# Kernel optimization log

Measured on AMD Instinct MI355X. Metric: run time of the kernel, lower is better.

The kernel has to match this reference:

```python
import jax, jax.numpy as jnp
import numpy as np
from jax import lax

N_THETAS = 16
N_RHOS = 5
N_BINS = N_THETAS * N_RHOS  # 80
N_FEAT = 4
N_ROT = 16
MAX_RHO = 12.0
EPS = 1e-5
N_SAMPLES = 4096
N_VERT = 128


def _initial_coords():
    grid_rho = np.linspace(0.0, MAX_RHO, num=N_RHOS + 1)[1:]
    grid_theta = np.linspace(0.0, 2 * np.pi, num=N_THETAS + 1)[:-1]
    gr, gt = np.meshgrid(grid_rho, grid_theta, sparse=False)
    gr = gr.T.flatten().astype(np.float32)  # [80]
    gt = gt.T.flatten().astype(np.float32)  # [80]
    return gr, gt


def setup_inputs() -> dict:
    key = jax.random.key(0)
    k1, k2, k3, k4, k5 = jax.random.split(key, 5)
    rho_coords = jax.random.uniform(k1, (N_SAMPLES, N_VERT), jnp.float32) * MAX_RHO
    theta_coords = jax.random.uniform(k2, (N_SAMPLES, N_VERT), jnp.float32) * (2 * np.pi)
    input_feat = jax.random.normal(k3, (N_SAMPLES, N_VERT, N_FEAT), jnp.float32)
    mask = (jax.random.uniform(k4, (N_SAMPLES, N_VERT, 1), jnp.float32) < 0.9).astype(jnp.float32)
    gr, gt = _initial_coords()
    mu_rho = jnp.tile(jnp.asarray(gr)[None, None, :], (N_FEAT, 1, 1))       # [F,1,80]
    mu_theta = jnp.tile(jnp.asarray(gt)[None, None, :], (N_FEAT, 1, 1))     # [F,1,80]
    sigma_rho = jnp.full((N_FEAT, 1, N_BINS), MAX_RHO / 8.0, jnp.float32)
    sigma_theta = jnp.ones((N_FEAT, 1, N_BINS), jnp.float32)
    # VarianceScaling(fan_avg, uniform) for square [80,80]: limit = sqrt(3/80)
    limit = np.sqrt(3.0 / N_BINS)
    W_conv = jax.random.uniform(k5, (N_FEAT, N_BINS, N_BINS), jnp.float32, -limit, limit)
    b_conv = jnp.zeros((N_FEAT, N_BINS), jnp.float32)
    return {
        "rho_coords": rho_coords, "theta_coords": theta_coords,
        "input_feat": input_feat, "mask": mask,
        "mu_rho": mu_rho, "sigma_rho": sigma_rho,
        "mu_theta": mu_theta, "sigma_theta": sigma_theta,
        "W_conv": W_conv, "b_conv": b_conv,
    }


def _geodesic_conv(rho_coords, theta_coords, input_feat, mask,
                   mu_rho, sigma_rho, mu_theta, sigma_theta, W_conv, b_conv):
    two_pi = jnp.float32(2 * np.pi)
    rot_step = two_pi / N_ROT
    outs = []
    for i in range(N_FEAT):  # small, structurally distinct feature channels
        feat = input_feat[:, :, i]  # [N,V]
        # rho Gaussian is rotation-independent: [N,V,80]
        rho_g = jnp.exp(-jnp.square(rho_coords[..., None] - mu_rho[i, 0])
                        / (jnp.square(sigma_rho[i, 0]) + EPS))
        init = jnp.full((rho_coords.shape[0], N_BINS), -jnp.inf, jnp.float32)

        def step(carry, k):
            th = jnp.mod(theta_coords + k * rot_step, two_pi)  # [N,V]
            th_g = jnp.exp(-jnp.square(th[..., None] - mu_theta[i, 0])
                           / (jnp.square(sigma_theta[i, 0]) + EPS))  # [N,V,80]
            g = rho_g * th_g * mask  # [N,V,80]
            g = g / (jnp.sum(g, axis=1, keepdims=True) + EPS)  # mean over patch
            desc = jnp.einsum('nvb,nv->nb', g, feat)  # [N,80]
            conv = desc @ W_conv[i] + b_conv[i]
            return jnp.maximum(carry, conv), None

        max_conv, _ = lax.scan(step, init, jnp.arange(N_ROT, dtype=jnp.float32))
        outs.append(jax.nn.relu(max_conv))
    return jnp.stack(outs, axis=1)  # [N, F, 80]


def reference(rho_coords, theta_coords, input_feat, mask,
              mu_rho, sigma_rho, mu_theta, sigma_theta, W_conv, b_conv):
    return _geodesic_conv(rho_coords, theta_coords, input_feat, mask,
                          mu_rho, sigma_rho, mu_theta, sigma_theta, W_conv, b_conv)
```

## Files before the change

kernel.cpp:

```cpp
#include <hip/hip_runtime.h>
#include <math.h>

#define NBINS 80
#define NVERT 128
#define NRH 5
#define NDEG 6

#define PSTR 136
#define VSTR 32
#define DSTR 80

#define OFF_VT 6800
#define VTSZ   6144
#define OFF_GM 19088
#define OFF_CNT 19344
#define SLICE  19360

#define NSET_C 48
#define NSET_W 60
#define WS_BYTES ((NSET_C + NSET_W) * 64 * 8 * 2)

typedef _Float16 half8 __attribute__((ext_vector_type(8)));
typedef float f32x4 __attribute__((ext_vector_type(4)));

__global__ __launch_bounds__(64) void prep_frags(const float* __restrict__ Wc,
                                                 const float* __restrict__ sig_th,
                                                 _Float16* __restrict__ ws) {
    const int blk  = blockIdx.x;
    const int lane = threadIdx.x;
    constexpr float TWO_PI = 6.28318530717958647692f;
    constexpr float DLT    = TWO_PI / 16.0f;
    constexpr float LN2    = 0.69314718055994530942f;
    half8 h;
    if (blk < NSET_C) {
        constexpr float LOG2E = 1.44269504088896340736f;
        constexpr float EPSF  = 1e-5f;
        const float st = sig_th[0];
        const float Kt = -LOG2E / (st * st + EPSF);
        const int ks = blk % 3;
        const int nt = blk / 3;
        const int t  = lane & 15;
        const int q  = lane >> 4;
        #pragma unroll
        for (int j = 0; j < 8; ++j) {
            const int k = ks * 32 + q * 8 + j;
            const int a = k / NDEG;
            const int d = k % NDEG;
            const int m = ((a + nt) & 15) - t;
            const float s = fmaf((float)m, DLT, 0.5f * DLT);
            const float z = 2.0f * LN2 * Kt * s * (0.5f * DLT);
            float val = exp2f(Kt * s * s);
            for (int dd = 1; dd <= d; ++dd) val *= z / (float)dd;
            h[j] = (_Float16)val;
        }
    } else {
        const int e    = blk - NSET_C;
        const int ks   = e % 3;
        const int tile = (e / 3) % 5;
        const int i    = e / 15;
        const int cc   = tile * 16 + (lane & 15);
        const int bb0  = ks * 32 + (lane >> 4) * 8;
        #pragma unroll
        for (int j = 0; j < 8; ++j) {
            const int bb = bb0 + j;
            h[j] = (_Float16)((bb < NBINS) ? Wc[i * NBINS * NBINS + bb * NBINS + cc] : 0.0f);
        }
    }
    *(half8*)(ws + ((size_t)blk * 64 + lane) * 8) = h;
}

template <int USEWS>
__global__ __launch_bounds__(128) void masif_geo_conv(
    const float* __restrict__ rho_c,
    const float* __restrict__ th_c,
    const float* __restrict__ feat_g,
    const float* __restrict__ mask_g,
    const float* __restrict__ mu_rho,
    const float* __restrict__ sig_rho,
    const float* __restrict__ mu_th,
    const float* __restrict__ sig_th,
    const float* __restrict__ Wc,
    const float* __restrict__ bcv,
    const _Float16* __restrict__ ws,
    const int nsamp,
    float* __restrict__ out)
{
    const int tid  = threadIdx.x;
    const int wave = tid >> 6;
    const int lane = tid & 63;
    const int n    = blockIdx.x;

    const int t  = lane & 15;
    const int kq = lane >> 4;

    __shared__ __align__(16) char s_raw[SLICE];
    _Float16* s_PM = (_Float16*)(s_raw);
    _Float16* s_vtw = (_Float16*)(s_raw + OFF_VT + wave * VTSZ);
    _Float16* s_gm = (_Float16*)(s_raw + OFF_GM);
    int*      s_cnt = (int*)(s_raw + OFF_CNT);
    _Float16* s_d  = (_Float16*)(s_raw);

    constexpr float LOG2E   = 1.44269504088896340736f;
    constexpr float TWO_PI  = 6.28318530717958647692f;
    constexpr float DLT     = TWO_PI / 16.0f;
    constexpr float INV_DLT = 16.0f / TWO_PI;
    constexpr float EPSF    = 1e-5f;

    const float st = sig_th[0];
    const float Kt = -LOG2E / (st * st + EPSF);
    const float sr = sig_rho[0];
    const float Kr = -LOG2E / (sr * sr + EPSF);
    float mr[NRH];
    #pragma unroll
    for (int r = 0; r < NRH; ++r) mr[r] = mu_rho[r * 16];

    #pragma unroll
    for (int x = 0; x < 4; ++x) {
        const int idx = x * 128 + tid;
        if (idx < 425) ((int4*)s_PM)[idx] = make_int4(0, 0, 0, 0);
    }

    const int v = wave * 64 + lane;
    const float  m   = mask_g[n * NVERT + v];
    const float  th0 = th_c[n * NVERT + v];
    const float  rho = rho_c[n * NVERT + v];
    const float4 f4  = *(const float4*)&feat_g[(n * NVERT + v) * 4];
    const bool act = (m != 0.0f);
    const unsigned long long bal = __ballot(act);
    if (lane == 0) s_cnt[wave] = (int)__popcll(bal);
    __syncthreads();
    const int base = wave ? s_cnt[0] : 0;
    const int nc   = s_cnt[0] + s_cnt[1];
    if (act) {
        const int pos = base + (int)__popcll(bal & ((1ull << lane) - 1ull));
        int aa = (int)floorf(th0 * INV_DLT);
        aa = aa > 15 ? 15 : (aa < 0 ? 0 : aa);
        const float rvp = th0 - (float)aa * DLT - 0.5f * DLT;
        float R[NRH];
        #pragma unroll
        for (int r = 0; r < NRH; ++r) {
            const float dr = rho - mr[r];
            R[r] = m * exp2f(Kr * dr * dr);
        }
        const float fv[4] = {f4.x, f4.y, f4.z, f4.w};
        #pragma unroll
        for (int f = 0; f < 4; ++f) {
            #pragma unroll
            for (int r = 0; r < 4; ++r)
                s_PM[(f * 4 + r) * PSTR + pos] = (_Float16)(fv[f] * R[r]);
            s_PM[(16 + f) * PSTR + pos] = (_Float16)(fv[f] * R[4]);
        }
        #pragma unroll
        for (int r = 0; r < NRH; ++r)
            s_PM[(20 + r) * PSTR + pos] = (_Float16)R[r];
        s_PM[(pos >> 3) * PSTR + 128 + (pos & 7)] = (_Float16)(rvp * (2.0f * INV_DLT));
        ((char*)s_PM)[(16 + (pos >> 4)) * 2 * PSTR + 256 + (pos & 15)] = (char)aa;
        s_gm[pos] = (_Float16)exp2f(Kt * rvp * rvp);
    }
    __syncthreads();

    f32x4 M[NDEG];
    #pragma unroll
    for (int ct = 0; ct < NDEG; ++ct) M[ct] = (f32x4){0.f, 0.f, 0.f, 0.f};
    const int arow = wave ? (16 + t) : t;
    const int nch = (nc + 31) >> 5;
    #pragma unroll 1
    for (int ch = 0; ch < nch; ++ch) {
        #pragma unroll
        for (int x = 0; x < 6; ++x)
            ((int4*)s_vtw)[x * 64 + lane] = make_int4(0, 0, 0, 0);
        {
            const int cl = lane >> 1;
            const int cg = ch * 32 + cl;
            if (cg < nc) {
                const float u = (float)s_PM[(cg >> 3) * PSTR + 128 + (cg & 7)];
                const float g = (float)s_gm[cg];
                const int   a = (int)((char*)s_PM)[(16 + (cg >> 4)) * 2 * PSTR + 256 + (cg & 15)];
                const int  dh = (lane & 1) * 3;
                float p0, p1, p2;
                if (dh == 0) { p0 = 1.0f; p1 = u; p2 = u * u; }
                else { const float u2 = u * u; p0 = u2 * u; p1 = u2 * u2; p2 = p0 * u2; }
                const int bi = (a * NDEG + dh) * VSTR + cl;
                s_vtw[bi]            = (_Float16)(g * p0);
                s_vtw[bi + VSTR]     = (_Float16)(g * p1);
                s_vtw[bi + 2 * VSTR] = (_Float16)(g * p2);
            }
        }
        const half8 a = *(const half8*)(s_PM + arow * PSTR + ch * 32 + kq * 8);
        #pragma unroll
        for (int ct = 0; ct < NDEG; ++ct) {
            const half8 b = *(const half8*)(s_vtw + (ct * 16 + t) * VSTR + kq * 8);
            M[ct] = __builtin_amdgcn_mfma_f32_16x16x32_f16(a, b, M[ct], 0, 0, 0);
        }
    }

    #pragma unroll
    for (int ct = 0; ct < NDEG; ++ct) {
        const int md = ct * 16 + t;
        #pragma unroll
        for (int reg = 0; reg < 4; ++reg) {
            const int lr = kq * 4 + reg;
            if (wave == 0)
                s_PM[lr * PSTR + md] = (_Float16)M[ct][reg];
            else if (lr < 9)
                s_PM[(16 + lr) * PSTR + md] = (_Float16)M[ct][reg];
        }
    }
    __syncthreads();

    half8 A0[3], A1[3];
    #pragma unroll
    for (int ks = 0; ks < 3; ++ks) {
        A0[ks] = *(const half8*)(s_PM + t * PSTR + ks * 32 + kq * 8);
        A1[ks] = *(const half8*)(s_PM + (16 + t) * PSTR + ks * 32 + kq * 8);
    }

    const half8* wsv = (const half8*)ws;
    #pragma unroll 1
    for (int gg = 0; gg < 2; ++gg) {
        const int g = wave * 2 + gg;
        f32x4 C0g[4], C1g[4];
        #pragma unroll
        for (int j = 0; j < 4; ++j) {
            C0g[j] = (f32x4){0.f, 0.f, 0.f, 0.f};
            C1g[j] = (f32x4){0.f, 0.f, 0.f, 0.f};
        }
        #pragma unroll
        for (int j = 0; j < 4; ++j) {
            const int nt = g * 4 + j;
            half8 b0, b1, b2;
            if (USEWS) {
                b0 = wsv[(size_t)((nt * 3 + 0) * 64 + lane)];
                b1 = wsv[(size_t)((nt * 3 + 1) * 64 + lane)];
                b2 = wsv[(size_t)((nt * 3 + 2) * 64 + lane)];
            } else {
                #pragma unroll
                for (int ks = 0; ks < 3; ++ks) {
                    half8 bb;
                    #pragma unroll
                    for (int jj = 0; jj < 8; ++jj) {
                        const int k = ks * 32 + kq * 8 + jj;
                        const int a = k / NDEG, d = k % NDEG;
                        const int mm = ((a + nt) & 15) - t;
                        const float s = fmaf((float)mm, DLT, 0.5f * DLT);
                        const float z = 2.0f * 0.69314718055994530942f * Kt * s * (0.5f * DLT);
                        float val = exp2f(Kt * s * s);
                        for (int dd = 1; dd <= d; ++dd) val *= z / (float)dd;
                        bb[jj] = (_Float16)val;
                    }
                    if (ks == 0) b0 = bb; else if (ks == 1) b1 = bb; else b2 = bb;
                }
            }
            C0g[j] = __builtin_amdgcn_mfma_f32_16x16x32_f16(A0[0], b0, C0g[j], 0, 0, 0);
            C1g[j] = __builtin_amdgcn_mfma_f32_16x16x32_f16(A1[0], b0, C1g[j], 0, 0, 0);
            C0g[j] = __builtin_amdgcn_mfma_f32_16x16x32_f16(A0[1], b1, C0g[j], 0, 0, 0);
            C1g[j] = __builtin_amdgcn_mfma_f32_16x16x32_f16(A1[1], b1, C1g[j], 0, 0, 0);
            C0g[j] = __builtin_amdgcn_mfma_f32_16x16x32_f16(A0[2], b2, C0g[j], 0, 0, 0);
            C1g[j] = __builtin_amdgcn_mfma_f32_16x16x32_f16(A1[2], b2, C1g[j], 0, 0, 0);
        }
        #pragma unroll
        for (int j = 0; j < 4; ++j) {
            const int nt = g * 4 + j;
            float den[5], inv[5];
            #pragma unroll
            for (int r = 0; r < 4; ++r) den[r] = __shfl(C1g[j][r], 16 + t);
            den[4] = __shfl(C1g[j][0], 32 + t);
            #pragma unroll
            for (int r = 0; r < NRH; ++r) {
                const float x = den[r] + EPSF;
                float vv = __builtin_amdgcn_rcpf(x);
                inv[r] = vv * (2.0f - x * vv);
            }
            #pragma unroll
            for (int reg = 0; reg < 4; ++reg)
                s_d[kq * 1280 + nt * DSTR + reg * 16 + t] =
                    (_Float16)(C0g[j][reg] * inv[reg]);
            if (kq == 0) {
                #pragma unroll
                for (int reg = 0; reg < 4; ++reg)
                    s_d[reg * 1280 + nt * DSTR + 64 + t] =
                        (_Float16)(C1g[j][reg] * inv[4]);
            }
        }
    }
    __syncthreads();

    #pragma unroll 1
    for (int ii = 0; ii < 2; ++ii) {
        const int i = wave * 2 + ii;
        f32x4 Cc[5];
        #pragma unroll
        for (int tile = 0; tile < 5; ++tile) Cc[tile] = (f32x4){0.f, 0.f, 0.f, 0.f};
        #pragma unroll
        for (int ks = 0; ks < 3; ++ks) {
            const half8 a = *(const half8*)(s_d + i * 1280 + t * DSTR + ks * 32 + kq * 8);
            #pragma unroll
            for (int tile = 0; tile < 5; ++tile) {
                half8 b;
                if (USEWS) {
                    b = wsv[(size_t)((NSET_C + (i * 5 + tile) * 3 + ks) * 64 + lane)];
                } else {
                    const int cc  = tile * 16 + t;
                    const int bb0 = ks * 32 + kq * 8;
                    #pragma unroll
                    for (int j = 0; j < 8; ++j) {
                        const int bb = bb0 + j;
                        b[j] = (_Float16)((bb < NBINS) ? Wc[i * NBINS * NBINS + bb * NBINS + cc] : 0.0f);
                    }
                }
                Cc[tile] = __builtin_amdgcn_mfma_f32_16x16x32_f16(a, b, Cc[tile], 0, 0, 0);
            }
        }
        #pragma unroll
        for (int tile = 0; tile < 5; ++tile) {
            float mx = fmaxf(fmaxf(Cc[tile][0], Cc[tile][1]), fmaxf(Cc[tile][2], Cc[tile][3]));
            mx = fmaxf(mx, __shfl_xor(mx, 16));
            mx = fmaxf(mx, __shfl_xor(mx, 32));
            if (lane < 16) {
                const int cc = tile * 16 + lane;
                out[(size_t)n * 320 + i * NBINS + cc] =
                    fmaxf(mx + bcv[i * NBINS + cc], 0.0f);
            }
        }
    }
}

extern "C" void kernel_launch(void* const* d_in, const int* in_sizes, int n_in,
                              void* d_out, int out_size, void* d_ws, size_t ws_size,
                              hipStream_t stream) {
    const float* rho   = (const float*)d_in[0];
    const float* theta = (const float*)d_in[1];
    const float* feat  = (const float*)d_in[2];
    const float* mask  = (const float*)d_in[3];
    const float* mu_r  = (const float*)d_in[4];
    const float* sg_r  = (const float*)d_in[5];
    const float* mu_t  = (const float*)d_in[6];
    const float* sg_t  = (const float*)d_in[7];
    const float* W     = (const float*)d_in[8];
    const float* bconv = (const float*)d_in[9];
    float* outp = (float*)d_out;

    const int nsamp = in_sizes[0] / NVERT;
    const int useWs = (ws_size >= (size_t)WS_BYTES) ? 1 : 0;
    _Float16* wsh = (_Float16*)d_ws;

    if (useWs) {
        prep_frags<<<NSET_C + NSET_W, 64, 0, stream>>>(W, sg_t, wsh);
        masif_geo_conv<1><<<nsamp, 128, 0, stream>>>(
            rho, theta, feat, mask, mu_r, sg_r, mu_t, sg_t, W, bconv,
            wsh, nsamp, outp);
    } else {
        masif_geo_conv<0><<<nsamp, 128, 0, stream>>>(
            rho, theta, feat, mask, mu_r, sg_r, mu_t, sg_t, W, bconv,
            wsh, nsamp, outp);
    }
}
```

Measured before the change: 124.6 us.

## Split per-sample work across four waves instead of two

Raises the block from 128 to 256 threads so each sample is handled by four waves. The first GEMM now splits its six column tiles by theta-bin half, so each wave builds a smaller Vandermonde slice. The later stages drop their per-wave two-iteration loops and give one feature channel to each wave. This adds a barrier and leaves two waves idle during the vertex load, but should shorten each sample's serial chain and raise wave-level parallelism.

```diff
diff --git a/kernel.cpp b/kernel.cpp
--- a/kernel.cpp
+++ b/kernel.cpp
@@ -11,7 +11,7 @@
 #define DSTR 80
 
 #define OFF_VT 6800
-#define VTSZ   6144
+#define VTSZ   3072
 #define OFF_GM 19088
 #define OFF_CNT 19344
 #define SLICE  19360
@@ -70,7 +70,7 @@
 }
 
 template <int USEWS>
-__global__ __launch_bounds__(128) void masif_geo_conv(
+__global__ __launch_bounds__(256) void masif_geo_conv(
     const float* __restrict__ rho_c,
     const float* __restrict__ th_c,
     const float* __restrict__ feat_g,
@@ -94,11 +94,11 @@
     const int kq = lane >> 4;
 
     __shared__ __align__(16) char s_raw[SLICE];
-    _Float16* s_PM = (_Float16*)(s_raw);
+    _Float16* s_PM  = (_Float16*)(s_raw);
     _Float16* s_vtw = (_Float16*)(s_raw + OFF_VT + wave * VTSZ);
-    _Float16* s_gm = (_Float16*)(s_raw + OFF_GM);
+    _Float16* s_gm  = (_Float16*)(s_raw + OFF_GM);
     int*      s_cnt = (int*)(s_raw + OFF_CNT);
-    _Float16* s_d  = (_Float16*)(s_raw);
+    _Float16* s_d   = (_Float16*)(s_raw);
 
     constexpr float LOG2E   = 1.44269504088896340736f;
     constexpr float TWO_PI  = 6.28318530717958647692f;
@@ -115,32 +115,38 @@
     for (int r = 0; r < NRH; ++r) mr[r] = mu_rho[r * 16];
 
     #pragma unroll
-    for (int x = 0; x < 4; ++x) {
-        const int idx = x * 128 + tid;
+    for (int x = 0; x < 2; ++x) {
+        const int idx = x * 256 + tid;
         if (idx < 425) ((int4*)s_PM)[idx] = make_int4(0, 0, 0, 0);
     }
 
-    const int v = wave * 64 + lane;
-    const float  m   = mask_g[n * NVERT + v];
-    const float  th0 = th_c[n * NVERT + v];
-    const float  rho = rho_c[n * NVERT + v];
-    const float4 f4  = *(const float4*)&feat_g[(n * NVERT + v) * 4];
-    const bool act = (m != 0.0f);
-    const unsigned long long bal = __ballot(act);
-    if (lane == 0) s_cnt[wave] = (int)__popcll(bal);
-    __syncthreads();
-    const int base = wave ? s_cnt[0] : 0;
-    const int nc   = s_cnt[0] + s_cnt[1];
+    bool act = false;
+    unsigned long long bal = 0;
+    float mv = 0.f, thv = 0.f, rhov = 0.f;
+    float4 f4 = make_float4(0.f, 0.f, 0.f, 0.f);
+    if (wave < 2) {
+        const int v = wave * 64 + lane;
+        mv   = mask_g[n * NVERT + v];
+        thv  = th_c[n * NVERT + v];
+        rhov = rho_c[n * NVERT + v];
+        f4   = *(const float4*)&feat_g[(n * NVERT + v) * 4];
+        act  = (mv != 0.0f);
+        bal  = __ballot(act);
+        if (lane == 0) s_cnt[wave] = (int)__popcll(bal);
+    }
+    __syncthreads();
+    const int nc = s_cnt[0] + s_cnt[1];
     if (act) {
+        const int base = wave ? s_cnt[0] : 0;
         const int pos = base + (int)__popcll(bal & ((1ull << lane) - 1ull));
-        int aa = (int)floorf(th0 * INV_DLT);
+        int aa = (int)floorf(thv * INV_DLT);
         aa = aa > 15 ? 15 : (aa < 0 ? 0 : aa);
-        const float rvp = th0 - (float)aa * DLT - 0.5f * DLT;
+        const float rvp = thv - (float)aa * DLT - 0.5f * DLT;
         float R[NRH];
         #pragma unroll
         for (int r = 0; r < NRH; ++r) {
-            const float dr = rho - mr[r];
-            R[r] = m * exp2f(Kr * dr * dr);
+            const float dr = rhov - mr[r];
+            R[r] = mv * exp2f(Kr * dr * dr);
         }
         const float fv[4] = {f4.x, f4.y, f4.z, f4.w};
         #pragma unroll
@@ -159,51 +165,55 @@
     }
     __syncthreads();
 
-    f32x4 M[NDEG];
-    #pragma unroll
-    for (int ct = 0; ct < NDEG; ++ct) M[ct] = (f32x4){0.f, 0.f, 0.f, 0.f};
-    const int arow = wave ? (16 + t) : t;
+    const int tile  = wave & 1;
+    const int chalf = wave >> 1;
+    f32x4 M[3];
+    #pragma unroll
+    for (int lct = 0; lct < 3; ++lct) M[lct] = (f32x4){0.f, 0.f, 0.f, 0.f};
+    const int arow = tile ? (16 + t) : t;
     const int nch = (nc + 31) >> 5;
     #pragma unroll 1
     for (int ch = 0; ch < nch; ++ch) {
         #pragma unroll
-        for (int x = 0; x < 6; ++x)
+        for (int x = 0; x < 3; ++x)
             ((int4*)s_vtw)[x * 64 + lane] = make_int4(0, 0, 0, 0);
         {
             const int cl = lane >> 1;
             const int cg = ch * 32 + cl;
             if (cg < nc) {
-                const float u = (float)s_PM[(cg >> 3) * PSTR + 128 + (cg & 7)];
-                const float g = (float)s_gm[cg];
-                const int   a = (int)((char*)s_PM)[(16 + (cg >> 4)) * 2 * PSTR + 256 + (cg & 15)];
-                const int  dh = (lane & 1) * 3;
-                float p0, p1, p2;
-                if (dh == 0) { p0 = 1.0f; p1 = u; p2 = u * u; }
-                else { const float u2 = u * u; p0 = u2 * u; p1 = u2 * u2; p2 = p0 * u2; }
-                const int bi = (a * NDEG + dh) * VSTR + cl;
-                s_vtw[bi]            = (_Float16)(g * p0);
-                s_vtw[bi + VSTR]     = (_Float16)(g * p1);
-                s_vtw[bi + 2 * VSTR] = (_Float16)(g * p2);
-            }
-        }
-        const half8 a = *(const half8*)(s_PM + arow * PSTR + ch * 32 + kq * 8);
-        #pragma unroll
-        for (int ct = 0; ct < NDEG; ++ct) {
-            const half8 b = *(const half8*)(s_vtw + (ct * 16 + t) * VSTR + kq * 8);
-            M[ct] = __builtin_amdgcn_mfma_f32_16x16x32_f16(a, b, M[ct], 0, 0, 0);
-        }
-    }
-
-    #pragma unroll
-    for (int ct = 0; ct < NDEG; ++ct) {
-        const int md = ct * 16 + t;
+                const int a = (int)((char*)s_PM)[(16 + (cg >> 4)) * 2 * PSTR + 256 + (cg & 15)];
+                if ((a >> 3) == chalf) {
+                    const float u = (float)s_PM[(cg >> 3) * PSTR + 128 + (cg & 7)];
+                    const float g = (float)s_gm[cg];
+                    const int  dh = (lane & 1) * 3;
+                    float p0, p1, p2;
+                    if (dh == 0) { p0 = 1.0f; p1 = u; p2 = u * u; }
+                    else { const float u2 = u * u; p0 = u2 * u; p1 = u2 * u2; p2 = p0 * u2; }
+                    const int bi = ((a - 8 * chalf) * NDEG + dh) * VSTR + cl;
+                    s_vtw[bi]            = (_Float16)(g * p0);
+                    s_vtw[bi + VSTR]     = (_Float16)(g * p1);
+                    s_vtw[bi + 2 * VSTR] = (_Float16)(g * p2);
+                }
+            }
+        }
+        const half8 av = *(const half8*)(s_PM + arow * PSTR + ch * 32 + kq * 8);
+        #pragma unroll
+        for (int lct = 0; lct < 3; ++lct) {
+            const half8 b = *(const half8*)(s_vtw + (lct * 16 + t) * VSTR + kq * 8);
+            M[lct] = __builtin_amdgcn_mfma_f32_16x16x32_f16(av, b, M[lct], 0, 0, 0);
+        }
+    }
+
+    #pragma unroll
+    for (int lct = 0; lct < 3; ++lct) {
+        const int md = (chalf * 3 + lct) * 16 + t;
         #pragma unroll
         for (int reg = 0; reg < 4; ++reg) {
             const int lr = kq * 4 + reg;
-            if (wave == 0)
-                s_PM[lr * PSTR + md] = (_Float16)M[ct][reg];
+            if (tile == 0)
+                s_PM[lr * PSTR + md] = (_Float16)M[lct][reg];
             else if (lr < 9)
-                s_PM[(16 + lr) * PSTR + md] = (_Float16)M[ct][reg];
+                s_PM[(16 + lr) * PSTR + md] = (_Float16)M[lct][reg];
         }
     }
     __syncthreads();
@@ -214,11 +224,11 @@
         A0[ks] = *(const half8*)(s_PM + t * PSTR + ks * 32 + kq * 8);
         A1[ks] = *(const half8*)(s_PM + (16 + t) * PSTR + ks * 32 + kq * 8);
     }
+    __syncthreads();
 
     const half8* wsv = (const half8*)ws;
-    #pragma unroll 1
-    for (int gg = 0; gg < 2; ++gg) {
-        const int g = wave * 2 + gg;
+    {
+        const int g = wave;
         f32x4 C0g[4], C1g[4];
         #pragma unroll
         for (int j = 0; j < 4; ++j) {
@@ -285,22 +295,21 @@
     }
     __syncthreads();
 
-    #pragma unroll 1
-    for (int ii = 0; ii < 2; ++ii) {
-        const int i = wave * 2 + ii;
+    {
+        const int i = wave;
         f32x4 Cc[5];
         #pragma unroll
-        for (int tile = 0; tile < 5; ++tile) Cc[tile] = (f32x4){0.f, 0.f, 0.f, 0.f};
+        for (int tl = 0; tl < 5; ++tl) Cc[tl] = (f32x4){0.f, 0.f, 0.f, 0.f};
         #pragma unroll
         for (int ks = 0; ks < 3; ++ks) {
             const half8 a = *(const half8*)(s_d + i * 1280 + t * DSTR + ks * 32 + kq * 8);
             #pragma unroll
-            for (int tile = 0; tile < 5; ++tile) {
+            for (int tl = 0; tl < 5; ++tl) {
                 half8 b;
                 if (USEWS) {
-                    b = wsv[(size_t)((NSET_C + (i * 5 + tile) * 3 + ks) * 64 + lane)];
+                    b = wsv[(size_t)((NSET_C + (i * 5 + tl) * 3 + ks) * 64 + lane)];
                 } else {
-                    const int cc  = tile * 16 + t;
+                    const int cc  = tl * 16 + t;
                     const int bb0 = ks * 32 + kq * 8;
                     #pragma unroll
                     for (int j = 0; j < 8; ++j) {
@@ -308,16 +317,16 @@
                         b[j] = (_Float16)((bb < NBINS) ? Wc[i * NBINS * NBINS + bb * NBINS + cc] : 0.0f);
                     }
                 }
-                Cc[tile] = __builtin_amdgcn_mfma_f32_16x16x32_f16(a, b, Cc[tile], 0, 0, 0);
-            }
-        }
-        #pragma unroll
-        for (int tile = 0; tile < 5; ++tile) {
-            float mx = fmaxf(fmaxf(Cc[tile][0], Cc[tile][1]), fmaxf(Cc[tile][2], Cc[tile][3]));
+                Cc[tl] = __builtin_amdgcn_mfma_f32_16x16x32_f16(a, b, Cc[tl], 0, 0, 0);
+            }
+        }
+        #pragma unroll
+        for (int tl = 0; tl < 5; ++tl) {
+            float mx = fmaxf(fmaxf(Cc[tl][0], Cc[tl][1]), fmaxf(Cc[tl][2], Cc[tl][3]));
             mx = fmaxf(mx, __shfl_xor(mx, 16));
             mx = fmaxf(mx, __shfl_xor(mx, 32));
             if (lane < 16) {
-                const int cc = tile * 16 + lane;
+                const int cc = tl * 16 + lane;
                 out[(size_t)n * 320 + i * NBINS + cc] =
                     fmaxf(mx + bcv[i * NBINS + cc], 0.0f);
             }
@@ -346,11 +355,11 @@
 
     if (useWs) {
         prep_frags<<<NSET_C + NSET_W, 64, 0, stream>>>(W, sg_t, wsh);
-        masif_geo_conv<1><<<nsamp, 128, 0, stream>>>(
+        masif_geo_conv<1><<<nsamp, 256, 0, stream>>>(
             rho, theta, feat, mask, mu_r, sg_r, mu_t, sg_t, W, bconv,
             wsh, nsamp, outp);
     } else {
-        masif_geo_conv<0><<<nsamp, 128, 0, stream>>>(
+        masif_geo_conv<0><<<nsamp, 256, 0, stream>>>(
             rho, theta, feat, mask, mu_r, sg_r, mu_t, sg_t, W, bconv,
             wsh, nsamp, outp);
     }
```

After: 118.4 us. 1.05x faster.
